# Performance work log

Hardware: AMD Instinct MI355X
Metric: run time of the kernel (lower is better)

The kernel has to match this reference:

```python
import jax, jax.numpy as jnp
import numpy as np

DIM = 4096
NH = 32
NKV = 8
HD = DIM // NH          # 128
REP = NH // NKV          # 4
B = 1
T = 2048
THETA = 500000.0
NEG = -1e9


def setup_inputs() -> dict:
    key = jax.random.key(0)
    ks = jax.random.split(key, 6)
    x = jax.random.normal(ks[0], (B, T, DIM), jnp.float32)
    # RoPE tables (real/imag parts of freqs_cis = exp(i * t * inv_freq))
    inv_freq = 1.0 / (THETA ** (np.arange(0, HD, 2, dtype=np.float32) / HD))  # (HD/2,)
    ang = np.outer(np.arange(T, dtype=np.float32), inv_freq)                  # (T, HD/2)
    freqs_cos = jnp.asarray(np.cos(ang), jnp.float32)
    freqs_sin = jnp.asarray(np.sin(ang), jnp.float32)
    # additive causal mask for prefill (pos=0): (T, T)
    mask = jnp.where(np.tril(np.ones((T, T), dtype=bool)), 0.0, NEG).astype(jnp.float32)
    cache_k = jnp.zeros((B, T, NKV, HD), jnp.float32)
    cache_v = jnp.zeros((B, T, NKV, HD), jnp.float32)
    s = 0.02
    wk_w = jax.random.normal(ks[1], (NKV * HD, DIM), jnp.float32) * s
    wk_b = jnp.zeros((NKV * HD,), jnp.float32)
    wv_w = jax.random.normal(ks[2], (NKV * HD, DIM), jnp.float32) * s
    wv_b = jnp.zeros((NKV * HD,), jnp.float32)
    wo_w = jax.random.normal(ks[3], (DIM, DIM), jnp.float32) * s
    wo_b = jnp.zeros((DIM,), jnp.float32)
    return dict(x=x, freqs_cos=freqs_cos, freqs_sin=freqs_sin, mask=mask,
                cache_k=cache_k, cache_v=cache_v,
                wk_w=wk_w, wk_b=wk_b, wv_w=wv_w, wv_b=wv_b,
                wo_w=wo_w, wo_b=wo_b, pos=0)


def _rope(t, cos, sin):
    # t: (B, T, H, HD); pairs (even, odd) form complex numbers
    tr = t.reshape(*t.shape[:-1], HD // 2, 2)
    re, im = tr[..., 0], tr[..., 1]
    c = cos[None, :, None, :]
    s = sin[None, :, None, :]
    out = jnp.stack([re * c - im * s, re * s + im * c], axis=-1)
    return out.reshape(t.shape)


def reference(x, freqs_cos, freqs_sin, mask, cache_k, cache_v,
              wk_w, wk_b, wv_w, wv_b, wo_w, wo_b, pos):
    Bx, Tx, D = x.shape
    # NOTE: faithful to source bug -- q projection uses wo (shared with output proj)
    q = x @ wo_w.T + wo_b                        # (B, T, D)
    k = x @ wk_w.T + wk_b                        # (B, T, NKV*HD)
    v = x @ wv_w.T + wv_b
    q = q.reshape(Bx, Tx, NH, HD)
    k = k.reshape(Bx, Tx, NKV, HD)
    v = v.reshape(Bx, Tx, NKV, HD)
    q = _rope(q, freqs_cos, freqs_sin)
    k = _rope(k, freqs_cos, freqs_sin)
    # KV-cache append then read back [:pos+T]
    ck = cache_k.at[:Bx, pos:pos + Tx].set(k)
    cv = cache_v.at[:Bx, pos:pos + Tx].set(v)
    k = ck[:Bx, :pos + Tx]
    v = cv[:Bx, :pos + Tx]
    # repeat_kv (GQA expansion)
    k = jnp.repeat(k, REP, axis=2)               # (B, S, NH, HD)
    v = jnp.repeat(v, REP, axis=2)
    scale = 1.0 / jnp.sqrt(jnp.float32(HD))
    scores = jnp.einsum('bqhd,bkhd->bhqk', q, k) * scale
    scores = scores + mask[None, None, :, :]
    p = jax.nn.softmax(scores.astype(jnp.float32), axis=-1)
    out = jnp.einsum('bhqk,bkhd->bqhd', p, v).reshape(Bx, Tx, D)
    return out @ wo_w.T + wo_b
```

## Files before the change

### kernel.cpp

```cpp
#include <hip/hip_runtime.h>
#include <stdint.h>
#include <stddef.h>

#define T_SEQ 2048
#define DIM   4096
#define NH    32
#define NKV   8
#define HD    128
#define KVD   (NKV*HD)

typedef __attribute__((ext_vector_type(8))) short short8;
typedef __attribute__((ext_vector_type(4))) float floatx4;
typedef __attribute__((ext_vector_type(2))) unsigned int uintx2;

static __device__ __forceinline__ float bf2f(short u) {
    union { unsigned int i; float f; } c; c.i = ((unsigned int)(unsigned short)u) << 16; return c.f;
}
static __device__ __forceinline__ short f2bf(float f) {
    union { float f; unsigned int u; } c; c.f = f;
    unsigned int r = c.u + 0x7fff + ((c.u >> 16) & 1);
    return (short)(r >> 16);
}
static __device__ __forceinline__ short8 ld8_f2b(const float* p) {
    floatx4 a = *(const floatx4*)p;
    floatx4 b = *(const floatx4*)(p + 4);
    short8 r;
    r[0]=f2bf(a[0]); r[1]=f2bf(a[1]); r[2]=f2bf(a[2]); r[3]=f2bf(a[3]);
    r[4]=f2bf(b[0]); r[5]=f2bf(b[1]); r[6]=f2bf(b[2]); r[7]=f2bf(b[3]);
    return r;
}

#define GLD16(g, l) __builtin_amdgcn_global_load_lds( \
    (const __attribute__((address_space(1))) unsigned int*)(g), \
    (__attribute__((address_space(3))) unsigned int*)(l), 16, 0, 0)

__global__ __launch_bounds__(256)
void cvt_bf16(const float* __restrict__ x, const float* __restrict__ wk,
              const float* __restrict__ wv, const float* __restrict__ wo,
              short* __restrict__ xb, short* __restrict__ wkb,
              short* __restrict__ wvb, short* __restrict__ wob) {
    size_t i8 = ((size_t)blockIdx.x * 256 + threadIdx.x) * 8;
    const float* src; short* dst; size_t off;
    if (i8 < 8388608)        { src = x;  dst = xb;  off = i8; }
    else if (i8 < 12582912)  { src = wk; dst = wkb; off = i8 - 8388608; }
    else if (i8 < 16777216)  { src = wv; dst = wvb; off = i8 - 12582912; }
    else                     { src = wo; dst = wob; off = i8 - 16777216; }
    *(short8*)(dst + off) = ld8_f2b(src + off);
}

template<bool C_F32>
static __device__ __forceinline__
void gemm_core(const short* __restrict__ A, const short* __restrict__ B,
               const float* __restrict__ bias, void* __restrict__ Cp,
               int N, int K, int bm, int bn) {
    __shared__ short sA0[128*32];
    __shared__ short sA1[128*32];
    __shared__ short sB0[128*32];
    __shared__ short sB1[128*32];
    const int tid  = threadIdx.x;
    const int wave = tid >> 6, lane = tid & 63;
    const int l15  = lane & 15, lq = lane >> 4;
    const int wm   = (wave >> 1) * 64, wn = (wave & 1) * 64;

    floatx4 acc[4][4];
    #pragma unroll
    for (int i = 0; i < 4; i++)
        #pragma unroll
        for (int j = 0; j < 4; j++)
            acc[i][j] = (floatx4)(0.0f);

    const int c0 = tid, c1 = 256 + tid;
    const int r0 = c0 >> 2, k0 = (c0 & 3) * 8;
    const int r1 = c1 >> 2, k1 = (c1 & 3) * 8;
    const short* pA0 = A + (size_t)(bm + r0) * K + k0;
    const short* pA1 = A + (size_t)(bm + r1) * K + k1;
    const short* pB0 = B + (size_t)(bn + r0) * K + k0;
    const short* pB1 = B + (size_t)(bn + r1) * K + k1;

    auto stage = [&](short* dA, short* dB, int kt) {
        GLD16(pA0 + kt, dA + c0 * 8);
        GLD16(pA1 + kt, dA + c1 * 8);
        GLD16(pB0 + kt, dB + c0 * 8);
        GLD16(pB1 + kt, dB + c1 * 8);
    };
    auto compute = [&](const short* dA, const short* dB) {
        short8 af[4], bfr[4];
        #pragma unroll
        for (int mi = 0; mi < 4; mi++)
            af[mi] = *(const short8*)&dA[(wm + mi*16 + l15)*32 + lq*8];
        #pragma unroll
        for (int ni = 0; ni < 4; ni++)
            bfr[ni] = *(const short8*)&dB[(wn + ni*16 + l15)*32 + lq*8];
        #pragma unroll
        for (int mi = 0; mi < 4; mi++)
            #pragma unroll
            for (int ni = 0; ni < 4; ni++)
                acc[mi][ni] = __builtin_amdgcn_mfma_f32_16x16x32_bf16(af[mi], bfr[ni], acc[mi][ni], 0, 0, 0);
    };

    stage(sA0, sB0, 0);
    __syncthreads();

    const int nt = K >> 5;
    for (int t = 0; t < nt; t += 2) {
        stage(sA1, sB1, (t + 1) * 32);
        compute(sA0, sB0);
        __syncthreads();
        if (t + 2 < nt) stage(sA0, sB0, (t + 2) * 32);
        compute(sA1, sB1);
        __syncthreads();
    }

    #pragma unroll
    for (int ni = 0; ni < 4; ni++) {
        int col = bn + wn + ni*16 + l15;
        float bv = bias[col];
        #pragma unroll
        for (int mi = 0; mi < 4; mi++) {
            int row = bm + wm + mi*16 + lq*4;
            #pragma unroll
            for (int r = 0; r < 4; r++) {
                float v = acc[mi][ni][r] + bv;
                if (C_F32) ((float*)Cp)[(size_t)(row + r)*N + col] = v;
                else       ((short*)Cp)[(size_t)(row + r)*N + col] = f2bf(v);
            }
        }
    }
}

template<bool C_F32>
__global__ __launch_bounds__(256)
void gemm_bt(const short* __restrict__ A, const short* __restrict__ B,
             const float* __restrict__ bias, void* __restrict__ Cp,
             int N, int K) {
    gemm_core<C_F32>(A, B, bias, Cp, N, K, blockIdx.y * 128, blockIdx.x * 128);
}

__global__ __launch_bounds__(256)
void gemm_kv(const short* __restrict__ A,
             const short* __restrict__ Bk, const float* __restrict__ bk, short* __restrict__ Ck,
             const short* __restrict__ Bv, const float* __restrict__ bv, short* __restrict__ Cv) {
    const short* B = blockIdx.z ? Bv : Bk;
    const float* bias = blockIdx.z ? bv : bk;
    short* C = blockIdx.z ? Cv : Ck;
    gemm_core<false>(A, B, bias, C, KVD, DIM, blockIdx.y * 128, blockIdx.x * 128);
}

#define QSC (0.08838834764831845f * 1.4426950408889634f)

__global__ __launch_bounds__(256)
void rope_k(short* __restrict__ Q, short* __restrict__ Kc,
            const float* __restrict__ fc, const float* __restrict__ fs) {
    int idx = blockIdx.x * 256 + threadIdx.x;
    const int NQ = T_SEQ * NH  * (HD/2);
    const int NK = T_SEQ * NKV * (HD/2);
    short* base; int t, i; size_t off; float sc;
    if (idx < NQ) {
        i = idx & 63;
        int th = idx >> 6;
        t = th >> 5;
        off = (size_t)th * HD + i*2;
        base = Q; sc = QSC;
    } else if (idx < NQ + NK) {
        int kidx = idx - NQ;
        i = kidx & 63;
        int th = kidx >> 6;
        t = th >> 3;
        off = (size_t)th * HD + i*2;
        base = Kc; sc = 1.0f;
    } else return;
    float re = bf2f(base[off]), im = bf2f(base[off+1]);
    float c = fc[t*64 + i], s = fs[t*64 + i];
    base[off]   = f2bf((re*c - im*s)*sc);
    base[off+1] = f2bf((re*s + im*c)*sc);
}

__global__ __launch_bounds__(256)
void vtrans(const short* __restrict__ V, short* __restrict__ Vt) {
    __shared__ short sT[64*72];
    const int tid = threadIdx.x;
    const int bt = blockIdx.x, bd = blockIdx.y;
    #pragma unroll
    for (int i = 0; i < 2; i++) {
        int c = i*256 + tid;
        int r = c >> 3, c8 = (c & 7) * 8;
        *(short8*)&sT[r*72 + c8] = *(const short8*)(V + (size_t)(bt*64 + r)*KVD + bd*64 + c8);
    }
    __syncthreads();
    #pragma unroll
    for (int i = 0; i < 2; i++) {
        int c = i*256 + tid;
        int d = c >> 3, t8 = (c & 7) * 8;
        short8 o;
        #pragma unroll
        for (int j = 0; j < 8; j++) o[j] = sT[(t8 + j)*72 + d];
        *(short8*)(Vt + (size_t)(bd*64 + d)*T_SEQ + bt*64 + t8) = o;
    }
}

__global__ __launch_bounds__(256, 2)
void flash_attn(const short* __restrict__ Q, const short* __restrict__ Kc,
                const short* __restrict__ Vt, short* __restrict__ O) {
    __shared__ short sK0[64*128];
    __shared__ short sK1[64*128];
    __shared__ short sV0[128*64];
    __shared__ short sV1[128*64];
    __shared__ short sP[4*2048];
    const int tid  = threadIdx.x;
    const int wave = tid >> 6, lane = tid & 63;
    const int l15  = lane & 15, lq = lane >> 4;
    const int sw   = l15 & 7;
    const int kvg  = blockIdx.y;
    const int qt   = (blockIdx.y < 4) ? (int)blockIdx.x : 63 - (int)blockIdx.x;
    const int hl   = wave;
    const int qb   = qt * 32;

    short8 qf[2][4];
    #pragma unroll
    for (int mi = 0; mi < 2; mi++)
        #pragma unroll
        for (int ks = 0; ks < 4; ks++)
            qf[mi][ks] = *(const short8*)(Q + (size_t)(qb + mi*16 + l15)*DIM
                                          + kvg*512 + hl*128 + ks*32 + lq*8);

    char* pw = (char*)(sP + wave*2048);

    int kc_r[4], kc_jg[4], vc_r[4], vc_jg[4];
    #pragma unroll
    for (int i = 0; i < 4; i++) {
        int c = i*256 + tid;
        kc_r[i]  = c >> 4;
        kc_jg[i] = (c & 15) ^ (kc_r[i] & 7);
        vc_r[i]  = c >> 3;
        vc_jg[i] = (c & 7) ^ (vc_r[i] & 7);
    }
    auto stage = [&](short* dK, short* dV, int kt) {
        #pragma unroll
        for (int i = 0; i < 4; i++) {
            int c = i*256 + tid;
            GLD16(Kc + (size_t)(kt*64 + kc_r[i])*KVD + kvg*HD + kc_jg[i]*8,
                  dK + c*8);
            GLD16(Vt + (size_t)(kvg*HD + vc_r[i])*T_SEQ + kt*64 + vc_jg[i]*8,
                  dV + c*8);
        }
    };

    float m_r[2] = {-1e30f, -1e30f};
    float l_r[2] = {0.0f, 0.0f};
    floatx4 o_acc[2][8];
    #pragma unroll
    for (int mi = 0; mi < 2; mi++)
        #pragma unroll
        for (int nd = 0; nd < 8; nd++) o_acc[mi][nd] = (floatx4)(0.0f);

    const int ktmax = qt >> 1;
    stage(sK0, sV0, 0);
    __syncthreads();

    for (int kt = 0; kt <= ktmax; kt++) {
        short* bK = (kt & 1) ? sK1 : sK0;
        short* bV = (kt & 1) ? sV1 : sV0;
        if (kt < ktmax) stage((kt & 1) ? sK0 : sK1, (kt & 1) ? sV0 : sV1, kt + 1);

        floatx4 s_acc[2][4];
        #pragma unroll
        for (int mi = 0; mi < 2; mi++)
            #pragma unroll
            for (int ni = 0; ni < 4; ni++) s_acc[mi][ni] = (floatx4)(0.0f);
        __builtin_amdgcn_s_setprio(1);
        #pragma unroll
        for (int ks = 0; ks < 4; ks++)
            #pragma unroll
            for (int ni = 0; ni < 4; ni++) {
                short8 kf = *(const short8*)&bK[(ni*16 + l15)*128
                                                + (((ks*4 + lq) ^ sw)*8)];
                s_acc[0][ni] = __builtin_amdgcn_mfma_f32_16x16x32_bf16(kf, qf[0][ks], s_acc[0][ni], 0, 0, 0);
                s_acc[1][ni] = __builtin_amdgcn_mfma_f32_16x16x32_bf16(kf, qf[1][ks], s_acc[1][ni], 0, 0, 0);
            }
        __builtin_amdgcn_s_setprio(0);

        const bool last = (kt == ktmax);

        #pragma unroll
        for (int mi = 0; mi < 2; mi++) {
            float sv[4][4];
            float mx = -1e30f;
            const int qrow = qb + mi*16 + l15;
            #pragma unroll
            for (int ni = 0; ni < 4; ni++)
                #pragma unroll
                for (int r = 0; r < 4; r++) {
                    float x = s_acc[mi][ni][r];
                    if (last) {
                        int kcol = kt*64 + ni*16 + lq*4 + r;
                        x = (kcol <= qrow) ? x : -1e30f;
                    }
                    sv[ni][r] = x;
                    mx = fmaxf(mx, x);
                }
            mx = fmaxf(mx, __shfl_xor(mx, 16));
            mx = fmaxf(mx, __shfl_xor(mx, 32));

            if (__any(mx - m_r[mi] > 8.0f)) {
                float mn = fmaxf(m_r[mi], mx);
                float a  = __builtin_amdgcn_exp2f(m_r[mi] - mn);
                m_r[mi] = mn;
                l_r[mi] *= a;
                float ar[4];
                #pragma unroll
                for (int r = 0; r < 4; r++) ar[r] = __shfl(a, lq*4 + r);
                #pragma unroll
                for (int nd = 0; nd < 8; nd++)
                    #pragma unroll
                    for (int r = 0; r < 4; r++) o_acc[mi][nd][r] *= ar[r];
            }

            float rs = 0.0f;
            #pragma unroll
            for (int ni = 0; ni < 4; ni++)
                #pragma unroll
                for (int r = 0; r < 4; r++) {
                    float p = __builtin_amdgcn_exp2f(sv[ni][r] - m_r[mi]);
                    sv[ni][r] = p;
                    rs += p;
                }
            rs += __shfl_xor(rs, 16);
            rs += __shfl_xor(rs, 32);
            l_r[mi] += rs;

            char* rowp = pw + (mi*16 + l15)*128 + (lq & 1)*8;
            #pragma unroll
            for (int ni = 0; ni < 4; ni++) {
                unsigned int lo, hi;
                asm("v_cvt_pk_bf16_f32 %0, %1, %2" : "=v"(lo) : "v"(sv[ni][0]), "v"(sv[ni][1]));
                asm("v_cvt_pk_bf16_f32 %0, %1, %2" : "=v"(hi) : "v"(sv[ni][2]), "v"(sv[ni][3]));
                int kc = ni*2 + (lq >> 1);
                *(uintx2*)(rowp + ((kc ^ sw) * 16)) = (uintx2){lo, hi};
            }
        }

        __builtin_amdgcn_s_setprio(1);
        #pragma unroll
        for (int ks = 0; ks < 2; ks++) {
            short8 pf[2];
            #pragma unroll
            for (int mi = 0; mi < 2; mi++)
                pf[mi] = *(const short8*)(pw + (mi*16 + l15)*128
                                          + (((ks*4 + lq) ^ sw)*16));
            #pragma unroll
            for (int nd = 0; nd < 8; nd++) {
                short8 vf = *(const short8*)&bV[(nd*16 + l15)*64
                                                + (((ks*4 + lq) ^ sw)*8)];
                o_acc[0][nd] = __builtin_amdgcn_mfma_f32_16x16x32_bf16(pf[0], vf, o_acc[0][nd], 0, 0, 0);
                o_acc[1][nd] = __builtin_amdgcn_mfma_f32_16x16x32_bf16(pf[1], vf, o_acc[1][nd], 0, 0, 0);
            }
        }
        __builtin_amdgcn_s_setprio(0);

        __syncthreads();
    }

    float rec[2][4];
    #pragma unroll
    for (int mi = 0; mi < 2; mi++) {
        float rv = 1.0f / l_r[mi];
        #pragma unroll
        for (int r = 0; r < 4; r++) rec[mi][r] = __shfl(rv, lq*4 + r);
    }
    #pragma unroll
    for (int mi = 0; mi < 2; mi++)
        #pragma unroll
        for (int nd = 0; nd < 8; nd++) {
            int col = (kvg*4 + hl)*HD + nd*16 + l15;
            #pragma unroll
            for (int r = 0; r < 4; r++) {
                int row = qb + mi*16 + lq*4 + r;
                O[(size_t)row*DIM + col] = f2bf(o_acc[mi][nd][r] * rec[mi][r]);
            }
        }
}

extern "C" void kernel_launch(void* const* d_in, const int* in_sizes, int n_in,
                              void* d_out, int out_size, void* d_ws, size_t ws_size,
                              hipStream_t stream) {
    const float* x    = (const float*)d_in[0];
    const float* fc   = (const float*)d_in[1];
    const float* fs   = (const float*)d_in[2];
    const float* wk_w = (const float*)d_in[6];
    const float* wk_b = (const float*)d_in[7];
    const float* wv_w = (const float*)d_in[8];
    const float* wv_b = (const float*)d_in[9];
    const float* wo_w = (const float*)d_in[10];
    const float* wo_b = (const float*)d_in[11];
    float* out = (float*)d_out;

    short* xb  = (short*)d_ws;
    short* wkb = xb  + 8388608;
    short* wvb = wkb + 4194304;
    short* wob = wvb + 4194304;
    short* Q   = wob + 16777216;
    short* K   = Q   + 8388608;
    short* V   = K   + 2097152;
    short* Vt  = V   + 2097152;
    short* AO  = Vt  + 2097152;

    cvt_bf16<<<dim3(16384), dim3(256), 0, stream>>>(x, wk_w, wv_w, wo_w, xb, wkb, wvb, wob);

    gemm_bt<false><<<dim3(32, 16), dim3(256), 0, stream>>>(xb, wob, wo_b, Q, DIM, DIM);
    gemm_kv<<<dim3(8, 16, 2), dim3(256), 0, stream>>>(xb, wkb, wk_b, K, wvb, wv_b, V);

    int nrope = T_SEQ*NH*(HD/2) + T_SEQ*NKV*(HD/2);
    rope_k<<<dim3((nrope + 255)/256), dim3(256), 0, stream>>>(Q, K, fc, fs);

    vtrans<<<dim3(32, 16), dim3(256), 0, stream>>>(V, Vt);

    flash_attn<<<dim3(64, 8), dim3(256), 0, stream>>>(Q, K, Vt, AO);

    gemm_bt<true><<<dim3(32, 16), dim3(256), 0, stream>>>(AO, wob, wo_b, out, DIM, DIM);
}
```

Measured before the change: 496.4 us.

## Triple-buffer GEMM LDS pipeline and fuse Q/K/V projections into one launch

The GEMM main loop moves from a double-buffered scheme with two full barriers per pair of k-tiles to a rotating triple buffer. It prefetches two tiles ahead, waits with a partial vmcnt, and uses a single barrier per iteration, so global loads overlap compute better. The Q projection and the K/V projection GEMMs are merged into one 48x16 grid launch. This removes a kernel boundary and improves CU fill, at the cost of 50% more LDS per block, which may lower occupancy. The vmcnt(4) wait assumes exactly four outstanding loads per stage, and correctness depends on that.

```diff
diff --git a/kernel.cpp b/kernel.cpp
--- a/kernel.cpp
+++ b/kernel.cpp
@@ -55,8 +55,10 @@
                int N, int K, int bm, int bn) {
     __shared__ short sA0[128*32];
     __shared__ short sA1[128*32];
+    __shared__ short sA2[128*32];
     __shared__ short sB0[128*32];
     __shared__ short sB1[128*32];
+    __shared__ short sB2[128*32];
     const int tid  = threadIdx.x;
     const int wave = tid >> 6, lane = tid & 63;
     const int l15  = lane & 15, lq = lane >> 4;
@@ -99,17 +101,24 @@
     };
 
     stage(sA0, sB0, 0);
-    __syncthreads();
+    stage(sA1, sB1, 32);
+    short *cA = sA0, *cB = sB0;
+    short *nA = sA1, *nB = sB1;
+    short *fA = sA2, *fB = sB2;
 
     const int nt = K >> 5;
-    for (int t = 0; t < nt; t += 2) {
-        stage(sA1, sB1, (t + 1) * 32);
-        compute(sA0, sB0);
-        __syncthreads();
-        if (t + 2 < nt) stage(sA0, sB0, (t + 2) * 32);
-        compute(sA1, sB1);
-        __syncthreads();
-    }
+    for (int t = 0; t < nt - 1; ++t) {
+        asm volatile("s_waitcnt vmcnt(4)" ::: "memory");
+        __builtin_amdgcn_s_barrier();
+        if (t + 2 < nt) stage(fA, fB, (t + 2) * 32);
+        compute(cA, cB);
+        short* x;
+        x = cA; cA = nA; nA = fA; fA = x;
+        x = cB; cB = nB; nB = fB; fB = x;
+    }
+    asm volatile("s_waitcnt vmcnt(0)" ::: "memory");
+    __builtin_amdgcn_s_barrier();
+    compute(cA, cB);
 
     #pragma unroll
     for (int ni = 0; ni < 4; ni++) {
@@ -137,13 +146,16 @@
 }
 
 __global__ __launch_bounds__(256)
-void gemm_kv(const short* __restrict__ A,
-             const short* __restrict__ Bk, const float* __restrict__ bk, short* __restrict__ Ck,
-             const short* __restrict__ Bv, const float* __restrict__ bv, short* __restrict__ Cv) {
-    const short* B = blockIdx.z ? Bv : Bk;
-    const float* bias = blockIdx.z ? bv : bk;
-    short* C = blockIdx.z ? Cv : Ck;
-    gemm_core<false>(A, B, bias, C, KVD, DIM, blockIdx.y * 128, blockIdx.x * 128);
+void gemm_qkv(const short* __restrict__ A,
+              const short* __restrict__ Bq, const float* __restrict__ bq, short* __restrict__ Cq,
+              const short* __restrict__ Bk, const float* __restrict__ bk, short* __restrict__ Ck,
+              const short* __restrict__ Bv, const float* __restrict__ bv, short* __restrict__ Cv) {
+    const int ct = blockIdx.x;
+    const short* B; const float* bias; short* C; int N, bn;
+    if (ct < 32)      { B = Bq; bias = bq; C = Cq; N = DIM; bn = ct*128; }
+    else if (ct < 40) { B = Bk; bias = bk; C = Ck; N = KVD; bn = (ct-32)*128; }
+    else              { B = Bv; bias = bv; C = Cv; N = KVD; bn = (ct-40)*128; }
+    gemm_core<false>(A, B, bias, C, N, DIM, blockIdx.y * 128, bn);
 }
 
 #define QSC (0.08838834764831845f * 1.4426950408889634f)
@@ -406,8 +418,8 @@
 
     cvt_bf16<<<dim3(16384), dim3(256), 0, stream>>>(x, wk_w, wv_w, wo_w, xb, wkb, wvb, wob);
 
-    gemm_bt<false><<<dim3(32, 16), dim3(256), 0, stream>>>(xb, wob, wo_b, Q, DIM, DIM);
-    gemm_kv<<<dim3(8, 16, 2), dim3(256), 0, stream>>>(xb, wkb, wk_b, K, wvb, wv_b, V);
+    gemm_qkv<<<dim3(48, 16), dim3(256), 0, stream>>>(
+        xb, wob, wo_b, Q, wkb, wk_b, K, wvb, wv_b, V);
 
     int nrope = T_SEQ*NH*(HD/2) + T_SEQ*NKV*(HD/2);
     rope_k<<<dim3((nrope + 255)/256), dim3(256), 0, stream>>>(Q, K, fc, fs);
```

New measurement: 487.3 us. No clear change (-1.8%).
